# Kernel tuning notes

Measured on AMD Instinct MI355X. Metric: run time of the kernel, lower is better.

Reference implementation:

```python
import jax, jax.numpy as jnp
import numpy as np

B, C_IN, C_OUT, H, W = 4, 64, 64, 64, 64
D = 2 * C_OUT  # projected channel dim = 128


def conv1x1(x, w, b):
    # x: [B,Cin,H,W], w: [Cout,Cin], b: [Cout]
    return jnp.einsum('bchw,oc->bohw', x, w) + b[None, :, None, None]


def setup_inputs() -> dict:
    key = jax.random.key(0)
    ks = jax.random.split(key, 10)
    s_q = 1.0 / np.sqrt(C_IN)
    s_kv = 1.0 / np.sqrt(2 * C_IN)
    s_o = 1.0 / np.sqrt(D)
    return {
        'x_upper': jax.random.normal(ks[0], (B, C_IN, H, W), jnp.float32),
        'x_lower': jax.random.normal(ks[1], (B, 2 * C_IN, H, W), jnp.float32),
        'wq': jax.random.uniform(ks[2], (D, C_IN), jnp.float32, -s_q, s_q),
        'bq': jax.random.uniform(ks[3], (D,), jnp.float32, -s_q, s_q),
        'wk': jax.random.uniform(ks[4], (D, 2 * C_IN), jnp.float32, -s_kv, s_kv),
        'bk': jax.random.uniform(ks[5], (D,), jnp.float32, -s_kv, s_kv),
        'wv': jax.random.uniform(ks[6], (D, 2 * C_IN), jnp.float32, -s_kv, s_kv),
        'bv': jax.random.uniform(ks[7], (D,), jnp.float32, -s_kv, s_kv),
        'wo': jax.random.uniform(ks[8], (D, D), jnp.float32, -s_o, s_o),
        'bo': jax.random.uniform(ks[9], (D,), jnp.float32, -s_o, s_o),
    }


def reference(x_upper, x_lower, wq, bq, wk, bk, wv, bv, wo, bo):
    q = conv1x1(x_upper, wq, bq)   # [B,D,H,W]
    k = conv1x1(x_lower, wk, bk)   # [B,D,H,W]
    v = conv1x1(x_lower, wv, bv)   # [B,D,H,W]
    b, d = q.shape[0], q.shape[1]
    # NOTE: the torch code uses .view (raw reshape), NOT a transpose --
    # faithful translation is a plain reshape of the contiguous NCHW tensor.
    qf = q.reshape(b, -1, d)       # [B, N, D], N = H*W
    kf = k.reshape(b, -1, d)
    vf = v.reshape(b, -1, d)
    scores = jnp.einsum('bnd,bmd->bnm', qf, kf) / (d ** 0.5)  # [B,N,N]
    attn = jax.nn.softmax(scores, axis=-1)
    of = jnp.einsum('bnm,bmd->bnd', attn, vf)  # [B,N,D]
    out = of.reshape(v.shape)                  # [B,D,H,W]
    out = conv1x1(out, wo, bo) + x_lower
    return out
```

## Files before the change

### kernel.cpp

```cpp
#include <hip/hip_runtime.h>
#include <math.h>

#define BB 4
#define CIN 64
#define CL 128
#define DD 128
#define HW 4096
#define NN 4096
#define TP 132
#define YP 136

typedef __attribute__((ext_vector_type(8))) __bf16 bf16x8;
typedef __attribute__((ext_vector_type(16))) float f32x16;

__device__ __forceinline__ unsigned short f2bf(float f) {
    unsigned u = __builtin_bit_cast(unsigned, f);
    u += 0x7fffu + ((u >> 16) & 1u);
    return (unsigned short)(u >> 16);
}
__device__ __forceinline__ unsigned pack2(float lo, float hi) {
    return (unsigned)f2bf(lo) | ((unsigned)f2bf(hi) << 16);
}
__device__ __forceinline__ float bf2f(unsigned s) {
    return __builtin_bit_cast(float, s << 16);
}
__device__ __forceinline__ unsigned pack_trunc(float lo, float hi) {
    return __builtin_amdgcn_perm(__builtin_bit_cast(unsigned, hi),
                                 __builtin_bit_cast(unsigned, lo), 0x07060302u);
}
__device__ __forceinline__ float exp2_fast(float x) {
#if __has_builtin(__builtin_amdgcn_exp2f)
    return __builtin_amdgcn_exp2f(x);
#else
    return __expf(x * 0.6931471805599453f);
#endif
}
__device__ __forceinline__ void async_copy16(const unsigned short* g,
                                             unsigned short* l) {
    __builtin_amdgcn_global_load_lds(
        (const __attribute__((address_space(1))) void*)g,
        (__attribute__((address_space(3))) void*)l, 16, 0, 0);
}

__device__ __forceinline__ void split8(const float xv[8], bf16x8* hi, bf16x8* lo) {
    union { unsigned u[4]; bf16x8 v; } H, L;
#pragma unroll
    for (int i = 0; i < 4; ++i) {
        float x0 = xv[2 * i], x1 = xv[2 * i + 1];
        H.u[i] = pack_trunc(x0, x1);
        float h0 = __builtin_bit_cast(float,
                     __builtin_bit_cast(unsigned, x0) & 0xffff0000u);
        float h1 = __builtin_bit_cast(float,
                     __builtin_bit_cast(unsigned, x1) & 0xffff0000u);
        L.u[i] = pack_trunc(x0 - h0, x1 - h1);
    }
    *hi = H.v; *lo = L.v;
}

__global__ __launch_bounds__(512) void proj_qkv_mfma(
    const float* __restrict__ xq, const float* __restrict__ wq,
    const float* __restrict__ bq, unsigned short* __restrict__ qout,
    const float* __restrict__ xl,
    const float* __restrict__ wk, const float* __restrict__ bk,
    const float* __restrict__ wv, const float* __restrict__ bv,
    unsigned short* __restrict__ kout, unsigned short* __restrict__ vout,
    float oscale)
{
    __shared__ __align__(16) char smem[135168];
    float* xsf = (float*)smem;
    unsigned short* ytk = (unsigned short*)(smem + 65536);
    unsigned short* ytv = (unsigned short*)(smem + 100352);

    const int tid = threadIdx.x;
    const int w = tid >> 6;
    const int lane = tid & 63;
    const int half = lane >> 5;
    const int l5 = lane & 31;

    if (blockIdx.x < 128) {
        const int b = blockIdx.x >> 5;
        const int tile = blockIdx.x & 31;
        const int px0 = tile * 128;
        const int g = w >> 2;
        const int ms = w & 3;

        {
            const float* src = xl + (size_t)b * CL * HW + px0
                             + (size_t)(lane >> 5) * HW + (lane & 31) * 4;
#pragma unroll
            for (int k = 0; k < 8; ++k) {
                int c = w * 8 + k;
                async_copy16((const unsigned short*)(src + (size_t)(2 * c) * HW),
                             (unsigned short*)(smem + c * 1024));
            }
        }

        const float* wsrc = g ? wv : wk;
        const float* bsrc = g ? bv : bk;
        bf16x8 Ah[8], Al[8];
        {
            const float* wr = wsrc + (size_t)(ms * 32 + l5) * CL + half * 8;
#pragma unroll
            for (int ks = 0; ks < 8; ++ks) {
                float tmp[8];
                *(float4*)&tmp[0] = *(const float4*)(wr + ks * 16);
                *(float4*)&tmp[4] = *(const float4*)(wr + ks * 16 + 4);
                split8(tmp, &Ah[ks], &Al[ks]);
            }
        }
        float biasr[16];
#pragma unroll
        for (int r = 0; r < 16; ++r)
            biasr[r] = bsrc[ms * 32 + (r & 3) + 8 * (r >> 2) + 4 * half];

        f32x16 acc[4];
#pragma unroll
        for (int ns = 0; ns < 4; ++ns)
#pragma unroll
            for (int r = 0; r < 16; ++r) acc[ns][r] = biasr[r];

        asm volatile("s_waitcnt vmcnt(0)" ::: "memory");
        __builtin_amdgcn_s_barrier();
        asm volatile("" ::: "memory");

#pragma unroll
        for (int ns = 0; ns < 4; ++ns) {
            int pxl = ns * 32 + l5;
#pragma unroll
            for (int ks = 0; ks < 8; ++ks) {
                int kb_ = ks * 16 + half * 8;
                float xv[8];
#pragma unroll
                for (int j = 0; j < 8; ++j)
                    xv[j] = xsf[(kb_ + j) * 128 + pxl];
                bf16x8 Bh, Bl;
                split8(xv, &Bh, &Bl);
                acc[ns] = __builtin_amdgcn_mfma_f32_32x32x16_bf16(Ah[ks], Bh, acc[ns], 0, 0, 0);
                acc[ns] = __builtin_amdgcn_mfma_f32_32x32x16_bf16(Ah[ks], Bl, acc[ns], 0, 0, 0);
                acc[ns] = __builtin_amdgcn_mfma_f32_32x32x16_bf16(Al[ks], Bh, acc[ns], 0, 0, 0);
            }
        }

        unsigned short* yt = g ? ytv : ytk;
#pragma unroll
        for (int ns = 0; ns < 4; ++ns) {
            int pxl = ns * 32 + l5;
#pragma unroll
            for (int r = 0; r < 16; ++r) {
                int o = ms * 32 + (r & 3) + 8 * (r >> 2) + 4 * half;
                yt[o * YP + pxl] = f2bf(acc[ns][r]);
            }
        }
        __syncthreads();

        unsigned short* kbase = kout + (size_t)b * NN * DD;
        unsigned short* vbase = vout + (size_t)b * 128 * HW + px0;
        const int tm = tile & 15;
#pragma unroll
        for (int i = 0; i < 4; ++i) {
            int e = tid + i * 512;
            int o = e >> 4, q = e & 15;
            uint4 kq4 = *(const uint4*)(ytk + o * YP + q * 8);
            *(uint4*)(kbase + (size_t)(o * 32 + tile) * 128 + ((q ^ tm) * 8)) = kq4;
            uint4 vq4 = *(const uint4*)(ytv + o * YP + q * 8);
            *(uint4*)(vbase + (size_t)o * HW + q * 8) = vq4;
        }
    } else {
        const int qb_ = blockIdx.x - 128;
        const int b = qb_ >> 5;
        const int tile = qb_ & 31;
        const int px0 = tile * 128;
        const int ms = w & 3;
        const int nsg = w >> 2;

        {
            const float* src = xq + (size_t)b * CIN * HW + px0
                             + (size_t)(lane >> 5) * HW + (lane & 31) * 4;
#pragma unroll
            for (int k = 0; k < 4; ++k) {
                int c = w * 4 + k;
                async_copy16((const unsigned short*)(src + (size_t)(2 * c) * HW),
                             (unsigned short*)(smem + c * 1024));
            }
        }

        bf16x8 Ah[4], Al[4];
        {
            const float* wr = wq + (size_t)(ms * 32 + l5) * CIN + half * 8;
#pragma unroll
            for (int ks = 0; ks < 4; ++ks) {
                float tmp[8];
                *(float4*)&tmp[0] = *(const float4*)(wr + ks * 16);
                *(float4*)&tmp[4] = *(const float4*)(wr + ks * 16 + 4);
                split8(tmp, &Ah[ks], &Al[ks]);
            }
        }
        float biasr[16];
#pragma unroll
        for (int r = 0; r < 16; ++r)
            biasr[r] = bq[ms * 32 + (r & 3) + 8 * (r >> 2) + 4 * half];

        f32x16 acc[2];
#pragma unroll
        for (int i = 0; i < 2; ++i)
#pragma unroll
            for (int r = 0; r < 16; ++r) acc[i][r] = biasr[r];

        asm volatile("s_waitcnt vmcnt(0)" ::: "memory");
        __builtin_amdgcn_s_barrier();
        asm volatile("" ::: "memory");

#pragma unroll
        for (int i = 0; i < 2; ++i) {
            int pxl = (nsg * 2 + i) * 32 + l5;
#pragma unroll
            for (int ks = 0; ks < 4; ++ks) {
                int kb_ = ks * 16 + half * 8;
                float xv[8];
#pragma unroll
                for (int j = 0; j < 8; ++j)
                    xv[j] = xsf[(kb_ + j) * 128 + pxl];
                bf16x8 Bh, Bl;
                split8(xv, &Bh, &Bl);
                acc[i] = __builtin_amdgcn_mfma_f32_32x32x16_bf16(Ah[ks], Bh, acc[i], 0, 0, 0);
                acc[i] = __builtin_amdgcn_mfma_f32_32x32x16_bf16(Ah[ks], Bl, acc[i], 0, 0, 0);
                acc[i] = __builtin_amdgcn_mfma_f32_32x32x16_bf16(Al[ks], Bh, acc[i], 0, 0, 0);
            }
        }

#pragma unroll
        for (int i = 0; i < 2; ++i) {
            int pxl = (nsg * 2 + i) * 32 + l5;
#pragma unroll
            for (int r = 0; r < 16; ++r) {
                int o = ms * 32 + (r & 3) + 8 * (r >> 2) + 4 * half;
                ytk[o * YP + pxl] = f2bf(acc[i][r] * oscale);
            }
        }
        __syncthreads();

        unsigned short* qbase = qout + (size_t)b * 128 * HW + px0;
#pragma unroll
        for (int i = 0; i < 4; ++i) {
            int e = tid + i * 512;
            int o = e >> 4, q = e & 15;
            uint4 qq4 = *(const uint4*)(ytk + o * YP + q * 8);
            *(uint4*)(qbase + (size_t)o * HW + q * 8) = qq4;
        }
    }
}

__global__ __launch_bounds__(512) void proj_o_mfma(
    const unsigned short* __restrict__ x, const float* __restrict__ w,
    const float* __restrict__ bias, const float* __restrict__ resid,
    float* __restrict__ out)
{
    __shared__ __align__(16) unsigned short xs16[128 * 64];

    const int tid = threadIdx.x;
    const int w_ = tid >> 6;
    const int lane = tid & 63;
    const int half = lane >> 5;
    const int l5 = lane & 31;
    const int b = blockIdx.x >> 6;
    const int tile = blockIdx.x & 63;
    const int px0 = tile * 64;
    const int ms = w_ & 3;
    const int pxh = w_ >> 2;

    {
        const unsigned short* src = x + (size_t)b * DD * HW + px0
                                  + (size_t)(lane >> 3) * HW + (lane & 7) * 8;
#pragma unroll
        for (int k = 0; k < 2; ++k) {
            int c = w_ * 2 + k;
            async_copy16(src + (size_t)(8 * c) * HW, xs16 + c * 512);
        }
    }

    bf16x8 Ah[8], Al[8];
    {
        const float* wr = w + (size_t)(ms * 32 + l5) * DD + half * 8;
#pragma unroll
        for (int ks = 0; ks < 8; ++ks) {
            float tmp[8];
            *(float4*)&tmp[0] = *(const float4*)(wr + ks * 16);
            *(float4*)&tmp[4] = *(const float4*)(wr + ks * 16 + 4);
            split8(tmp, &Ah[ks], &Al[ks]);
        }
    }
    f32x16 acc;
#pragma unroll
    for (int r = 0; r < 16; ++r)
        acc[r] = bias[ms * 32 + (r & 3) + 8 * (r >> 2) + 4 * half];

    asm volatile("s_waitcnt vmcnt(0)" ::: "memory");
    __builtin_amdgcn_s_barrier();
    asm volatile("" ::: "memory");

    {
        int pxl = pxh * 32 + l5;
#pragma unroll
        for (int ks = 0; ks < 8; ++ks) {
            int kb_ = ks * 16 + half * 8;
            union { unsigned u[4]; bf16x8 v; } B;
#pragma unroll
            for (int p = 0; p < 4; ++p) {
                unsigned e0 = xs16[(kb_ + 2 * p) * 64 + pxl];
                unsigned e1 = xs16[(kb_ + 2 * p + 1) * 64 + pxl];
                B.u[p] = e0 | (e1 << 16);
            }
            acc = __builtin_amdgcn_mfma_f32_32x32x16_bf16(Ah[ks], B.v, acc, 0, 0, 0);
            acc = __builtin_amdgcn_mfma_f32_32x32x16_bf16(Al[ks], B.v, acc, 0, 0, 0);
        }
    }

    {
        int px = px0 + pxh * 32 + l5;
#pragma unroll
        for (int r = 0; r < 16; ++r) {
            int o = ms * 32 + (r & 3) + 8 * (r >> 2) + 4 * half;
            size_t a = ((size_t)b * 128 + o) * HW + px;
            out[a] = acc[r] + resid[a];
        }
    }
}

__global__ __launch_bounds__(256) void transpose_v(
    const unsigned short* __restrict__ vf, unsigned short* __restrict__ vt)
{
    __shared__ unsigned short tld[16 * TP];
    int tid = threadIdx.x;
    int b = blockIdx.x >> 8;
    int n0 = (blockIdx.x & 255) * 16;
    const unsigned short* src = vf + (size_t)b * NN * DD + (size_t)n0 * DD;
    {
        int n = tid >> 4, x = tid & 15;
        union { uint4 q; unsigned long long u[2]; } t;
        t.q = *(const uint4*)(src + (size_t)n * DD + x * 8);
        unsigned short* d = &tld[n * TP + x * 8];
        *(unsigned long long*)(d) = t.u[0];
        *(unsigned long long*)(d + 4) = t.u[1];
    }
    __syncthreads();
    unsigned short* dst = vt + (size_t)b * NN * DD + (size_t)(n0 >> 7) * 16384;
    int xb_ = (n0 & 127) >> 3;
    {
        int g = tid & 1, d = tid >> 1;
        union { uint4 q; unsigned short s[8]; } t;
#pragma unroll
        for (int j = 0; j < 8; ++j) t.s[j] = tld[(g * 8 + j) * TP + d];
        int xs = (xb_ + g) ^ (d & 15);
        *(uint4*)(dst + (size_t)d * 128 + xs * 8) = t.q;
    }
}

__global__ __launch_bounds__(512) void attn_mfma(
    const unsigned short* __restrict__ qf, const unsigned short* __restrict__ kfs,
    const unsigned short* __restrict__ vts, unsigned short* __restrict__ of)
{
    __shared__ __align__(16) char smem[133632];

    const int tid = threadIdx.x;
    const int lane = tid & 63;
    const int w = tid >> 6;
    const int kq = w & 3;
    const int rh = w >> 2;
    const int half = lane >> 5;
    const int l5 = lane & 31;
    const int b = blockIdx.x >> 6;
    const int rb0 = (blockIdx.x & 63) * 64;
    const int rw0 = rb0 + rh * 32;
    const int cw = kq * 32;

    const unsigned short* qb = qf + (size_t)b * NN * DD;
    const unsigned short* kb = kfs + (size_t)b * NN * DD;
    const unsigned short* vb = vts + (size_t)b * NN * DD;

    bf16x8 qfrag[8];
    {
        const unsigned short* qrow = qb + (size_t)(rw0 + l5) * DD + half * 8;
#pragma unroll
        for (int kk = 0; kk < 8; ++kk)
            qfrag[kk] = *(const bf16x8*)(qrow + kk * 16);
    }

    f32x16 O[4] = {};
    float lacc = 0.f;

    auto stage = [&](int t, int buf) {
        const unsigned short* kt = kb + (size_t)t * 16384;
        const unsigned short* vt_ = vb + (size_t)t * 16384;
        unsigned short* kl = (unsigned short*)(smem + buf * 65536);
        unsigned short* vl = kl + 16384;
#pragma unroll
        for (int j = 0; j < 4; ++j) {
            int c = (w * 4 + j) * 512;
            async_copy16(kt + c + lane * 8, kl + c);
            async_copy16(vt_ + c + lane * 8, vl + c);
        }
    };

    stage(0, 0);
    stage(1, 1);

    const int NT = NN / 128;
    for (int t = 0; t < NT; ++t) {
        const int cur = t & 1;
        if (t < NT - 1) asm volatile("s_waitcnt vmcnt(8)" ::: "memory");
        else            asm volatile("s_waitcnt vmcnt(0)" ::: "memory");
        __builtin_amdgcn_s_barrier();
        asm volatile("" ::: "memory");

        const unsigned short* kl = (const unsigned short*)(smem + cur * 65536);
        const unsigned short* vl = kl + 16384;

        f32x16 S = {};
        __builtin_amdgcn_s_setprio(1);
#pragma unroll
        for (int kk = 0; kk < 8; ++kk) {
            bf16x8 kfr = *(const bf16x8*)
                &kl[(cw + l5) * 128 + (((kk * 2 + half) ^ (l5 & 15)) * 8)];
            S = __builtin_amdgcn_mfma_f32_32x32x16_bf16(kfr, qfrag[kk], S, 0, 0, 0);
        }
        __builtin_amdgcn_s_setprio(0);

        float p[16];
#pragma unroll
        for (int r = 0; r < 16; ++r) p[r] = exp2_fast(S[r]);
        {
            float t0 = (p[0] + p[1]) + (p[2] + p[3]);
            float t1 = (p[4] + p[5]) + (p[6] + p[7]);
            float t2 = (p[8] + p[9]) + (p[10] + p[11]);
            float t3 = (p[12] + p[13]) + (p[14] + p[15]);
            lacc += (t0 + t1) + (t2 + t3);
        }

#pragma unroll
        for (int kc = 0; kc < 2; ++kc) {
            unsigned PA0 = pack_trunc(p[8 * kc + 0], p[8 * kc + 1]);
            unsigned PA1 = pack_trunc(p[8 * kc + 2], p[8 * kc + 3]);
            unsigned PB0 = pack_trunc(p[8 * kc + 4], p[8 * kc + 5]);
            unsigned PB1 = pack_trunc(p[8 * kc + 6], p[8 * kc + 7]);
            unsigned snd0 = half ? PA0 : PB0;
            unsigned snd1 = half ? PA1 : PB1;
            unsigned rcv0 = (unsigned)__shfl_xor((int)snd0, 32, 64);
            unsigned rcv1 = (unsigned)__shfl_xor((int)snd1, 32, 64);
            union { unsigned u[4]; bf16x8 v; } pf;
            pf.u[0] = half ? rcv0 : PA0;
            pf.u[1] = half ? rcv1 : PA1;
            pf.u[2] = half ? PB0 : rcv0;
            pf.u[3] = half ? PB1 : rcv1;
            __builtin_amdgcn_s_setprio(1);
#pragma unroll
            for (int ds = 0; ds < 4; ++ds) {
                bf16x8 vfr = *(const bf16x8*)
                    &vl[(ds * 32 + l5) * 128 +
                        (((kq * 4 + kc * 2 + half) ^ (l5 & 15)) * 8)];
                O[ds] = __builtin_amdgcn_mfma_f32_32x32x16_bf16(vfr, pf.v, O[ds], 0, 0, 0);
            }
            __builtin_amdgcn_s_setprio(0);
        }

        asm volatile("s_waitcnt lgkmcnt(0)" ::: "memory");
        __builtin_amdgcn_s_barrier();
        asm volatile("" ::: "memory");
        if (t + 2 < NT) stage(t + 2, cur);
    }

    lacc += __shfl_xor(lacc, 32, 64);

    float (*red_o)[64][129] = (float (*)[64][129])smem;
    float* red_l = (float*)(smem + 132096);
    if (half == 0) red_l[kq * 64 + rh * 32 + l5] = lacc;
#pragma unroll
    for (int ds = 0; ds < 4; ++ds)
#pragma unroll
        for (int r = 0; r < 16; ++r) {
            int d = ds * 32 + (r & 3) + 8 * (r >> 2) + 4 * half;
            red_o[kq][rh * 32 + l5][d] = O[ds][r];
        }
    __syncthreads();

    {
        int q = tid >> 3;
        int dg = tid & 7;
        float l = red_l[q] + red_l[64 + q] + red_l[128 + q] + red_l[192 + q];
        float inv = 1.f / l;
        unsigned outw[8];
#pragma unroll
        for (int i = 0; i < 8; ++i) {
            int d0 = dg * 16 + i * 2;
            float s0 = red_o[0][q][d0] + red_o[1][q][d0] +
                       red_o[2][q][d0] + red_o[3][q][d0];
            float s1 = red_o[0][q][d0 + 1] + red_o[1][q][d0 + 1] +
                       red_o[2][q][d0 + 1] + red_o[3][q][d0 + 1];
            outw[i] = pack2(s0 * inv, s1 * inv);
        }
        unsigned short* ob = of + (size_t)b * NN * DD + (size_t)(rb0 + q) * DD + dg * 16;
        *(uint4*)(ob) = *(uint4*)&outw[0];
        *(uint4*)(ob + 8) = *(uint4*)&outw[4];
    }
}

extern "C" void kernel_launch(void* const* d_in, const int* in_sizes, int n_in,
                              void* d_out, int out_size, void* d_ws, size_t ws_size,
                              hipStream_t stream) {
    const float* x_upper = (const float*)d_in[0];
    const float* x_lower = (const float*)d_in[1];
    const float* wq = (const float*)d_in[2];
    const float* bq = (const float*)d_in[3];
    const float* wk = (const float*)d_in[4];
    const float* bk = (const float*)d_in[5];
    const float* wv = (const float*)d_in[6];
    const float* bv = (const float*)d_in[7];
    const float* wo = (const float*)d_in[8];
    const float* bo = (const float*)d_in[9];
    float* out = (float*)d_out;

    const size_t ELT = (size_t)BB * NN * DD;
    unsigned short* qf  = (unsigned short*)d_ws;
    unsigned short* kfs = qf + ELT;
    unsigned short* vts = kfs + ELT;
    unsigned short* vfn = vts + ELT;
    unsigned short* ofb = vfn + ELT;

    const float qscale = (float)(0.08838834764831845 * 1.4426950408889634);

    proj_qkv_mfma<<<256, 512, 0, stream>>>(x_upper, wq, bq, qf,
                                           x_lower, wk, bk, wv, bv,
                                           kfs, vfn, qscale);
    transpose_v<<<1024, 256, 0, stream>>>(vfn, vts);
    attn_mfma<<<BB * 64, 512, 0, stream>>>(qf, kfs, vts, ofb);
    proj_o_mfma<<<256, 512, 0, stream>>>(ofb, wo, bo, x_lower, out);
}
```

Measured before the change: 150.3 us.

## Fuse all four kernels into one cooperative kernel with grid syncs

Merges the QKV projection, V transpose, attention and output projection into a single cooperative launch of 256 blocks, separated by grid.sync barriers with threadfences. The transpose stage is remapped so each of the 256 blocks handles 64 rows instead of launching 1024 small blocks. The aim is to remove kernel launch gaps and per-kernel ramp overhead. In exchange, grid-wide barriers add synchronisation cost, and the large shared-memory footprint limits residency to one block per CU.

```diff
diff --git a/kernel.cpp b/kernel.cpp
--- a/kernel.cpp
+++ b/kernel.cpp
@@ -1,5 +1,8 @@
 #include <hip/hip_runtime.h>
+#include <hip/hip_cooperative_groups.h>
 #include <math.h>
+
+namespace cg = cooperative_groups;
 
 #define BB 4
 #define CIN 64
@@ -57,49 +60,410 @@
     *hi = H.v; *lo = L.v;
 }
 
-__global__ __launch_bounds__(512) void proj_qkv_mfma(
+__global__ __launch_bounds__(512) void fused_all(
     const float* __restrict__ xq, const float* __restrict__ wq,
     const float* __restrict__ bq, unsigned short* __restrict__ qout,
     const float* __restrict__ xl,
     const float* __restrict__ wk, const float* __restrict__ bk,
     const float* __restrict__ wv, const float* __restrict__ bv,
-    unsigned short* __restrict__ kout, unsigned short* __restrict__ vout,
-    float oscale)
+    unsigned short* __restrict__ kout, unsigned short* __restrict__ vfn,
+    unsigned short* __restrict__ vts, unsigned short* __restrict__ ofb,
+    const float* __restrict__ wo, const float* __restrict__ bo,
+    float* __restrict__ out, float oscale)
 {
     __shared__ __align__(16) char smem[135168];
-    float* xsf = (float*)smem;
-    unsigned short* ytk = (unsigned short*)(smem + 65536);
-    unsigned short* ytv = (unsigned short*)(smem + 100352);
-
+
+    cg::grid_group grid = cg::this_grid();
+    const int blk = blockIdx.x;
     const int tid = threadIdx.x;
-    const int w = tid >> 6;
-    const int lane = tid & 63;
-    const int half = lane >> 5;
-    const int l5 = lane & 31;
-
-    if (blockIdx.x < 128) {
-        const int b = blockIdx.x >> 5;
-        const int tile = blockIdx.x & 31;
-        const int px0 = tile * 128;
-        const int g = w >> 2;
-        const int ms = w & 3;
-
+
+    {
+        float* xsf = (float*)smem;
+        unsigned short* ytk = (unsigned short*)(smem + 65536);
+        unsigned short* ytv = (unsigned short*)(smem + 100352);
+        const int w = tid >> 6;
+        const int lane = tid & 63;
+        const int half = lane >> 5;
+        const int l5 = lane & 31;
+
+        if (blk < 128) {
+            const int b = blk >> 5;
+            const int tile = blk & 31;
+            const int px0 = tile * 128;
+            const int g = w >> 2;
+            const int ms = w & 3;
+
+            {
+                const float* src = xl + (size_t)b * CL * HW + px0
+                                 + (size_t)(lane >> 5) * HW + (lane & 31) * 4;
+#pragma unroll
+                for (int k = 0; k < 8; ++k) {
+                    int c = w * 8 + k;
+                    async_copy16((const unsigned short*)(src + (size_t)(2 * c) * HW),
+                                 (unsigned short*)(smem + c * 1024));
+                }
+            }
+
+            const float* wsrc = g ? wv : wk;
+            const float* bsrc = g ? bv : bk;
+            bf16x8 Ah[8], Al[8];
+            {
+                const float* wr = wsrc + (size_t)(ms * 32 + l5) * CL + half * 8;
+#pragma unroll
+                for (int ks = 0; ks < 8; ++ks) {
+                    float tmp[8];
+                    *(float4*)&tmp[0] = *(const float4*)(wr + ks * 16);
+                    *(float4*)&tmp[4] = *(const float4*)(wr + ks * 16 + 4);
+                    split8(tmp, &Ah[ks], &Al[ks]);
+                }
+            }
+            float biasr[16];
+#pragma unroll
+            for (int r = 0; r < 16; ++r)
+                biasr[r] = bsrc[ms * 32 + (r & 3) + 8 * (r >> 2) + 4 * half];
+
+            f32x16 acc[4];
+#pragma unroll
+            for (int ns = 0; ns < 4; ++ns)
+#pragma unroll
+                for (int r = 0; r < 16; ++r) acc[ns][r] = biasr[r];
+
+            asm volatile("s_waitcnt vmcnt(0)" ::: "memory");
+            __builtin_amdgcn_s_barrier();
+            asm volatile("" ::: "memory");
+
+#pragma unroll
+            for (int ns = 0; ns < 4; ++ns) {
+                int pxl = ns * 32 + l5;
+#pragma unroll
+                for (int ks = 0; ks < 8; ++ks) {
+                    int kb_ = ks * 16 + half * 8;
+                    float xv[8];
+#pragma unroll
+                    for (int j = 0; j < 8; ++j)
+                        xv[j] = xsf[(kb_ + j) * 128 + pxl];
+                    bf16x8 Bh, Bl;
+                    split8(xv, &Bh, &Bl);
+                    acc[ns] = __builtin_amdgcn_mfma_f32_32x32x16_bf16(Ah[ks], Bh, acc[ns], 0, 0, 0);
+                    acc[ns] = __builtin_amdgcn_mfma_f32_32x32x16_bf16(Ah[ks], Bl, acc[ns], 0, 0, 0);
+                    acc[ns] = __builtin_amdgcn_mfma_f32_32x32x16_bf16(Al[ks], Bh, acc[ns], 0, 0, 0);
+                }
+            }
+
+            unsigned short* yt = g ? ytv : ytk;
+#pragma unroll
+            for (int ns = 0; ns < 4; ++ns) {
+                int pxl = ns * 32 + l5;
+#pragma unroll
+                for (int r = 0; r < 16; ++r) {
+                    int o = ms * 32 + (r & 3) + 8 * (r >> 2) + 4 * half;
+                    yt[o * YP + pxl] = f2bf(acc[ns][r]);
+                }
+            }
+            __syncthreads();
+
+            unsigned short* kbase = kout + (size_t)b * NN * DD;
+            unsigned short* vbase = vfn + (size_t)b * 128 * HW + px0;
+            const int tm = tile & 15;
+#pragma unroll
+            for (int i = 0; i < 4; ++i) {
+                int e = tid + i * 512;
+                int o = e >> 4, q = e & 15;
+                uint4 kq4 = *(const uint4*)(ytk + o * YP + q * 8);
+                *(uint4*)(kbase + (size_t)(o * 32 + tile) * 128 + ((q ^ tm) * 8)) = kq4;
+                uint4 vq4 = *(const uint4*)(ytv + o * YP + q * 8);
+                *(uint4*)(vbase + (size_t)o * HW + q * 8) = vq4;
+            }
+        } else {
+            const int qb_ = blk - 128;
+            const int b = qb_ >> 5;
+            const int tile = qb_ & 31;
+            const int px0 = tile * 128;
+            const int ms = w & 3;
+            const int nsg = w >> 2;
+
+            {
+                const float* src = xq + (size_t)b * CIN * HW + px0
+                                 + (size_t)(lane >> 5) * HW + (lane & 31) * 4;
+#pragma unroll
+                for (int k = 0; k < 4; ++k) {
+                    int c = w * 4 + k;
+                    async_copy16((const unsigned short*)(src + (size_t)(2 * c) * HW),
+                                 (unsigned short*)(smem + c * 1024));
+                }
+            }
+
+            bf16x8 Ah[4], Al[4];
+            {
+                const float* wr = wq + (size_t)(ms * 32 + l5) * CIN + half * 8;
+#pragma unroll
+                for (int ks = 0; ks < 4; ++ks) {
+                    float tmp[8];
+                    *(float4*)&tmp[0] = *(const float4*)(wr + ks * 16);
+                    *(float4*)&tmp[4] = *(const float4*)(wr + ks * 16 + 4);
+                    split8(tmp, &Ah[ks], &Al[ks]);
+                }
+            }
+            float biasr[16];
+#pragma unroll
+            for (int r = 0; r < 16; ++r)
+                biasr[r] = bq[ms * 32 + (r & 3) + 8 * (r >> 2) + 4 * half];
+
+            f32x16 acc[2];
+#pragma unroll
+            for (int i = 0; i < 2; ++i)
+#pragma unroll
+                for (int r = 0; r < 16; ++r) acc[i][r] = biasr[r];
+
+            asm volatile("s_waitcnt vmcnt(0)" ::: "memory");
+            __builtin_amdgcn_s_barrier();
+            asm volatile("" ::: "memory");
+
+#pragma unroll
+            for (int i = 0; i < 2; ++i) {
+                int pxl = (nsg * 2 + i) * 32 + l5;
+#pragma unroll
+                for (int ks = 0; ks < 4; ++ks) {
+                    int kb_ = ks * 16 + half * 8;
+                    float xv[8];
+#pragma unroll
+                    for (int j = 0; j < 8; ++j)
+                        xv[j] = xsf[(kb_ + j) * 128 + pxl];
+                    bf16x8 Bh, Bl;
+                    split8(xv, &Bh, &Bl);
+                    acc[i] = __builtin_amdgcn_mfma_f32_32x32x16_bf16(Ah[ks], Bh, acc[i], 0, 0, 0);
+                    acc[i] = __builtin_amdgcn_mfma_f32_32x32x16_bf16(Ah[ks], Bl, acc[i], 0, 0, 0);
+                    acc[i] = __builtin_amdgcn_mfma_f32_32x32x16_bf16(Al[ks], Bh, acc[i], 0, 0, 0);
+                }
+            }
+
+#pragma unroll
+            for (int i = 0; i < 2; ++i) {
+                int pxl = (nsg * 2 + i) * 32 + l5;
+#pragma unroll
+                for (int r = 0; r < 16; ++r) {
+                    int o = ms * 32 + (r & 3) + 8 * (r >> 2) + 4 * half;
+                    ytk[o * YP + pxl] = f2bf(acc[i][r] * oscale);
+                }
+            }
+            __syncthreads();
+
+            unsigned short* qbase = qout + (size_t)b * 128 * HW + px0;
+#pragma unroll
+            for (int i = 0; i < 4; ++i) {
+                int e = tid + i * 512;
+                int o = e >> 4, q = e & 15;
+                uint4 qq4 = *(const uint4*)(ytk + o * YP + q * 8);
+                *(uint4*)(qbase + (size_t)o * HW + q * 8) = qq4;
+            }
+        }
+    }
+    __threadfence();
+    grid.sync();
+
+    {
+        unsigned short* tld = (unsigned short*)smem;
+        const int b = blk >> 6;
+        const int n0 = (blk & 63) * 64;
+        const unsigned short* src = vfn + (size_t)b * NN * DD + (size_t)n0 * DD;
+#pragma unroll
+        for (int i = 0; i < 2; ++i) {
+            int ch = tid + i * 512;
+            int n = ch >> 4, x = ch & 15;
+            union { uint4 q; unsigned long long u[2]; } t;
+            t.q = *(const uint4*)(src + (size_t)n * DD + x * 8);
+            unsigned short* d = &tld[n * TP + x * 8];
+            *(unsigned long long*)(d) = t.u[0];
+            *(unsigned long long*)(d + 4) = t.u[1];
+        }
+        __syncthreads();
+        unsigned short* dst = vts + (size_t)b * NN * DD + (size_t)(n0 >> 7) * 16384;
+        int xb_ = (n0 & 127) >> 3;
+#pragma unroll
+        for (int i = 0; i < 2; ++i) {
+            int ch = tid + i * 512;
+            int g = ch & 7, d = ch >> 3;
+            union { uint4 q; unsigned short s[8]; } t;
+#pragma unroll
+            for (int j = 0; j < 8; ++j) t.s[j] = tld[(g * 8 + j) * TP + d];
+            int xs = (xb_ + g) ^ (d & 15);
+            *(uint4*)(dst + (size_t)d * 128 + xs * 8) = t.q;
+        }
+        __syncthreads();
+    }
+    __threadfence();
+    grid.sync();
+
+    {
+        const int lane = tid & 63;
+        const int w = tid >> 6;
+        const int kq = w & 3;
+        const int rh = w >> 2;
+        const int half = lane >> 5;
+        const int l5 = lane & 31;
+        const int b = blk >> 6;
+        const int rb0 = (blk & 63) * 64;
+        const int rw0 = rb0 + rh * 32;
+        const int cw = kq * 32;
+
+        const unsigned short* qb = qout + (size_t)b * NN * DD;
+        const unsigned short* kb = kout + (size_t)b * NN * DD;
+        const unsigned short* vb = vts + (size_t)b * NN * DD;
+
+        bf16x8 qfrag[8];
         {
-            const float* src = xl + (size_t)b * CL * HW + px0
-                             + (size_t)(lane >> 5) * HW + (lane & 31) * 4;
-#pragma unroll
-            for (int k = 0; k < 8; ++k) {
-                int c = w * 8 + k;
-                async_copy16((const unsigned short*)(src + (size_t)(2 * c) * HW),
-                             (unsigned short*)(smem + c * 1024));
-            }
-        }
-
-        const float* wsrc = g ? wv : wk;
-        const float* bsrc = g ? bv : bk;
+            const unsigned short* qrow = qb + (size_t)(rw0 + l5) * DD + half * 8;
+#pragma unroll
+            for (int kk = 0; kk < 8; ++kk)
+                qfrag[kk] = *(const bf16x8*)(qrow + kk * 16);
+        }
+
+        f32x16 O[4] = {};
+        float lacc = 0.f;
+
+        auto stage = [&](int t, int buf) {
+            const unsigned short* kt = kb + (size_t)t * 16384;
+            const unsigned short* vt_ = vb + (size_t)t * 16384;
+            unsigned short* kl = (unsigned short*)(smem + buf * 65536);
+            unsigned short* vl = kl + 16384;
+#pragma unroll
+            for (int j = 0; j < 4; ++j) {
+                int c = (w * 4 + j) * 512;
+                async_copy16(kt + c + lane * 8, kl + c);
+                async_copy16(vt_ + c + lane * 8, vl + c);
+            }
+        };
+
+        stage(0, 0);
+        stage(1, 1);
+
+        const int NT = NN / 128;
+        for (int t = 0; t < NT; ++t) {
+            const int cur = t & 1;
+            if (t < NT - 1) asm volatile("s_waitcnt vmcnt(8)" ::: "memory");
+            else            asm volatile("s_waitcnt vmcnt(0)" ::: "memory");
+            __builtin_amdgcn_s_barrier();
+            asm volatile("" ::: "memory");
+
+            const unsigned short* kl = (const unsigned short*)(smem + cur * 65536);
+            const unsigned short* vl = kl + 16384;
+
+            f32x16 S = {};
+            __builtin_amdgcn_s_setprio(1);
+#pragma unroll
+            for (int kk = 0; kk < 8; ++kk) {
+                bf16x8 kfr = *(const bf16x8*)
+                    &kl[(cw + l5) * 128 + (((kk * 2 + half) ^ (l5 & 15)) * 8)];
+                S = __builtin_amdgcn_mfma_f32_32x32x16_bf16(kfr, qfrag[kk], S, 0, 0, 0);
+            }
+            __builtin_amdgcn_s_setprio(0);
+
+            float p[16];
+#pragma unroll
+            for (int r = 0; r < 16; ++r) p[r] = exp2_fast(S[r]);
+            {
+                float t0 = (p[0] + p[1]) + (p[2] + p[3]);
+                float t1 = (p[4] + p[5]) + (p[6] + p[7]);
+                float t2 = (p[8] + p[9]) + (p[10] + p[11]);
+                float t3 = (p[12] + p[13]) + (p[14] + p[15]);
+                lacc += (t0 + t1) + (t2 + t3);
+            }
+
+#pragma unroll
+            for (int kc = 0; kc < 2; ++kc) {
+                unsigned PA0 = pack_trunc(p[8 * kc + 0], p[8 * kc + 1]);
+                unsigned PA1 = pack_trunc(p[8 * kc + 2], p[8 * kc + 3]);
+                unsigned PB0 = pack_trunc(p[8 * kc + 4], p[8 * kc + 5]);
+                unsigned PB1 = pack_trunc(p[8 * kc + 6], p[8 * kc + 7]);
+                unsigned snd0 = half ? PA0 : PB0;
+                unsigned snd1 = half ? PA1 : PB1;
+                unsigned rcv0 = (unsigned)__shfl_xor((int)snd0, 32, 64);
+                unsigned rcv1 = (unsigned)__shfl_xor((int)snd1, 32, 64);
+                union { unsigned u[4]; bf16x8 v; } pf;
+                pf.u[0] = half ? rcv0 : PA0;
+                pf.u[1] = half ? rcv1 : PA1;
+                pf.u[2] = half ? PB0 : rcv0;
+                pf.u[3] = half ? PB1 : rcv1;
+                __builtin_amdgcn_s_setprio(1);
+#pragma unroll
+                for (int ds = 0; ds < 4; ++ds) {
+                    bf16x8 vfr = *(const bf16x8*)
+                        &vl[(ds * 32 + l5) * 128 +
+                            (((kq * 4 + kc * 2 + half) ^ (l5 & 15)) * 8)];
+                    O[ds] = __builtin_amdgcn_mfma_f32_32x32x16_bf16(vfr, pf.v, O[ds], 0, 0, 0);
+                }
+                __builtin_amdgcn_s_setprio(0);
+            }
+
+            asm volatile("s_waitcnt lgkmcnt(0)" ::: "memory");
+            __builtin_amdgcn_s_barrier();
+            asm volatile("" ::: "memory");
+            if (t + 2 < NT) stage(t + 2, cur);
+        }
+
+        lacc += __shfl_xor(lacc, 32, 64);
+
+        float (*red_o)[64][129] = (float (*)[64][129])smem;
+        float* red_l = (float*)(smem + 132096);
+        if (half == 0) red_l[kq * 64 + rh * 32 + l5] = lacc;
+#pragma unroll
+        for (int ds = 0; ds < 4; ++ds)
+#pragma unroll
+            for (int r = 0; r < 16; ++r) {
+                int d = ds * 32 + (r & 3) + 8 * (r >> 2) + 4 * half;
+                red_o[kq][rh * 32 + l5][d] = O[ds][r];
+            }
+        __syncthreads();
+
+        {
+            int q = tid >> 3;
+            int dg = tid & 7;
+            float l = red_l[q] + red_l[64 + q] + red_l[128 + q] + red_l[192 + q];
+            float inv = 1.f / l;
+            unsigned outw[8];
+#pragma unroll
+            for (int i = 0; i < 8; ++i) {
+                int d0 = dg * 16 + i * 2;
+                float s0 = red_o[0][q][d0] + red_o[1][q][d0] +
+                           red_o[2][q][d0] + red_o[3][q][d0];
+                float s1 = red_o[0][q][d0 + 1] + red_o[1][q][d0 + 1] +
+                           red_o[2][q][d0 + 1] + red_o[3][q][d0 + 1];
+                outw[i] = pack2(s0 * inv, s1 * inv);
+            }
+            unsigned short* ob = ofb + (size_t)b * NN * DD + (size_t)(rb0 + q) * DD + dg * 16;
+            *(uint4*)(ob) = *(uint4*)&outw[0];
+            *(uint4*)(ob + 8) = *(uint4*)&outw[4];
+        }
+        __syncthreads();
+    }
+    __threadfence();
+    grid.sync();
+
+    {
+        unsigned short* xs16 = (unsigned short*)smem;
+        const int w_ = tid >> 6;
+        const int lane = tid & 63;
+        const int half = lane >> 5;
+        const int l5 = lane & 31;
+        const int b = blk >> 6;
+        const int tile = blk & 63;
+        const int px0 = tile * 64;
+        const int ms = w_ & 3;
+        const int pxh = w_ >> 2;
+
+        {
+            const unsigned short* src = ofb + (size_t)b * DD * HW + px0
+                                      + (size_t)(lane >> 3) * HW + (lane & 7) * 8;
+#pragma unroll
+            for (int k = 0; k < 2; ++k) {
+                int c = w_ * 2 + k;
+                async_copy16(src + (size_t)(8 * c) * HW, xs16 + c * 512);
+            }
+        }
+
         bf16x8 Ah[8], Al[8];
         {
-            const float* wr = wsrc + (size_t)(ms * 32 + l5) * CL + half * 8;
+            const float* wr = wo + (size_t)(ms * 32 + l5) * DD + half * 8;
 #pragma unroll
             for (int ks = 0; ks < 8; ++ks) {
                 float tmp[8];
@@ -108,398 +472,41 @@
                 split8(tmp, &Ah[ks], &Al[ks]);
             }
         }
-        float biasr[16];
+        f32x16 acc;
 #pragma unroll
         for (int r = 0; r < 16; ++r)
-            biasr[r] = bsrc[ms * 32 + (r & 3) + 8 * (r >> 2) + 4 * half];
-
-        f32x16 acc[4];
-#pragma unroll
-        for (int ns = 0; ns < 4; ++ns)
-#pragma unroll
-            for (int r = 0; r < 16; ++r) acc[ns][r] = biasr[r];
+            acc[r] = bo[ms * 32 + (r & 3) + 8 * (r >> 2) + 4 * half];
 
         asm volatile("s_waitcnt vmcnt(0)" ::: "memory");
         __builtin_amdgcn_s_barrier();
         asm volatile("" ::: "memory");
 
-#pragma unroll
-        for (int ns = 0; ns < 4; ++ns) {
-            int pxl = ns * 32 + l5;
+        {
+            int pxl = pxh * 32 + l5;
 #pragma unroll
             for (int ks = 0; ks < 8; ++ks) {
                 int kb_ = ks * 16 + half * 8;
-                float xv[8];
-#pragma unroll
-                for (int j = 0; j < 8; ++j)
-                    xv[j] = xsf[(kb_ + j) * 128 + pxl];
-                bf16x8 Bh, Bl;
-                split8(xv, &Bh, &Bl);
-                acc[ns] = __builtin_amdgcn_mfma_f32_32x32x16_bf16(Ah[ks], Bh, acc[ns], 0, 0, 0);
-                acc[ns] = __builtin_amdgcn_mfma_f32_32x32x16_bf16(Ah[ks], Bl, acc[ns], 0, 0, 0);
-                acc[ns] = __builtin_amdgcn_mfma_f32_32x32x16_bf16(Al[ks], Bh, acc[ns], 0, 0, 0);
-            }
-        }
-
-        unsigned short* yt = g ? ytv : ytk;
-#pragma unroll
-        for (int ns = 0; ns < 4; ++ns) {
-            int pxl = ns * 32 + l5;
+                union { unsigned u[4]; bf16x8 v; } B;
+#pragma unroll
+                for (int p = 0; p < 4; ++p) {
+                    unsigned e0 = xs16[(kb_ + 2 * p) * 64 + pxl];
+                    unsigned e1 = xs16[(kb_ + 2 * p + 1) * 64 + pxl];
+                    B.u[p] = e0 | (e1 << 16);
+                }
+                acc = __builtin_amdgcn_mfma_f32_32x32x16_bf16(Ah[ks], B.v, acc, 0, 0, 0);
+                acc = __builtin_amdgcn_mfma_f32_32x32x16_bf16(Al[ks], B.v, acc, 0, 0, 0);
+            }
+        }
+
+        {
+            int px = px0 + pxh * 32 + l5;
 #pragma unroll
             for (int r = 0; r < 16; ++r) {
                 int o = ms * 32 + (r & 3) + 8 * (r >> 2) + 4 * half;
-                yt[o * YP + pxl] = f2bf(acc[ns][r]);
-            }
-        }
-        __syncthreads();
-
-        unsigned short* kbase = kout + (size_t)b * NN * DD;
-        unsigned short* vbase = vout + (size_t)b * 128 * HW + px0;
-        const int tm = tile & 15;
-#pragma unroll
-        for (int i = 0; i < 4; ++i) {
-            int e = tid + i * 512;
-            int o = e >> 4, q = e & 15;
-            uint4 kq4 = *(const uint4*)(ytk + o * YP + q * 8);
-            *(uint4*)(kbase + (size_t)(o * 32 + tile) * 128 + ((q ^ tm) * 8)) = kq4;
-            uint4 vq4 = *(const uint4*)(ytv + o * YP + q * 8);
-            *(uint4*)(vbase + (size_t)o * HW + q * 8) = vq4;
-        }
-    } else {
-        const int qb_ = blockIdx.x - 128;
-        const int b = qb_ >> 5;
-        const int tile = qb_ & 31;
-        const int px0 = tile * 128;
-        const int ms = w & 3;
-        const int nsg = w >> 2;
-
-        {
-            const float* src = xq + (size_t)b * CIN * HW + px0
-                             + (size_t)(lane >> 5) * HW + (lane & 31) * 4;
-#pragma unroll
-            for (int k = 0; k < 4; ++k) {
-                int c = w * 4 + k;
-                async_copy16((const unsigned short*)(src + (size_t)(2 * c) * HW),
-                             (unsigned short*)(smem + c * 1024));
-            }
-        }
-
-        bf16x8 Ah[4], Al[4];
-        {
-            const float* wr = wq + (size_t)(ms * 32 + l5) * CIN + half * 8;
-#pragma unroll
-            for (int ks = 0; ks < 4; ++ks) {
-                float tmp[8];
-                *(float4*)&tmp[0] = *(const float4*)(wr + ks * 16);
-                *(float4*)&tmp[4] = *(const float4*)(wr + ks * 16 + 4);
-                split8(tmp, &Ah[ks], &Al[ks]);
-            }
-        }
-        float biasr[16];
-#pragma unroll
-        for (int r = 0; r < 16; ++r)
-            biasr[r] = bq[ms * 32 + (r & 3) + 8 * (r >> 2) + 4 * half];
-
-        f32x16 acc[2];
-#pragma unroll
-        for (int i = 0; i < 2; ++i)
-#pragma unroll
-            for (int r = 0; r < 16; ++r) acc[i][r] = biasr[r];
-
-        asm volatile("s_waitcnt vmcnt(0)" ::: "memory");
-        __builtin_amdgcn_s_barrier();
-        asm volatile("" ::: "memory");
-
-#pragma unroll
-        for (int i = 0; i < 2; ++i) {
-            int pxl = (nsg * 2 + i) * 32 + l5;
-#pragma unroll
-            for (int ks = 0; ks < 4; ++ks) {
-                int kb_ = ks * 16 + half * 8;
-                float xv[8];
-#pragma unroll
-                for (int j = 0; j < 8; ++j)
-                    xv[j] = xsf[(kb_ + j) * 128 + pxl];
-                bf16x8 Bh, Bl;
-                split8(xv, &Bh, &Bl);
-                acc[i] = __builtin_amdgcn_mfma_f32_32x32x16_bf16(Ah[ks], Bh, acc[i], 0, 0, 0);
-                acc[i] = __builtin_amdgcn_mfma_f32_32x32x16_bf16(Ah[ks], Bl, acc[i], 0, 0, 0);
-                acc[i] = __builtin_amdgcn_mfma_f32_32x32x16_bf16(Al[ks], Bh, acc[i], 0, 0, 0);
-            }
-        }
-
-#pragma unroll
-        for (int i = 0; i < 2; ++i) {
-            int pxl = (nsg * 2 + i) * 32 + l5;
-#pragma unroll
-            for (int r = 0; r < 16; ++r) {
-                int o = ms * 32 + (r & 3) + 8 * (r >> 2) + 4 * half;
-                ytk[o * YP + pxl] = f2bf(acc[i][r] * oscale);
-            }
-        }
-        __syncthreads();
-
-        unsigned short* qbase = qout + (size_t)b * 128 * HW + px0;
-#pragma unroll
-        for (int i = 0; i < 4; ++i) {
-            int e = tid + i * 512;
-            int o = e >> 4, q = e & 15;
-            uint4 qq4 = *(const uint4*)(ytk + o * YP + q * 8);
-            *(uint4*)(qbase + (size_t)o * HW + q * 8) = qq4;
-        }
-    }
-}
-
-__global__ __launch_bounds__(512) void proj_o_mfma(
-    const unsigned short* __restrict__ x, const float* __restrict__ w,
-    const float* __restrict__ bias, const float* __restrict__ resid,
-    float* __restrict__ out)
-{
-    __shared__ __align__(16) unsigned short xs16[128 * 64];
-
-    const int tid = threadIdx.x;
-    const int w_ = tid >> 6;
-    const int lane = tid & 63;
-    const int half = lane >> 5;
-    const int l5 = lane & 31;
-    const int b = blockIdx.x >> 6;
-    const int tile = blockIdx.x & 63;
-    const int px0 = tile * 64;
-    const int ms = w_ & 3;
-    const int pxh = w_ >> 2;
-
-    {
-        const unsigned short* src = x + (size_t)b * DD * HW + px0
-                                  + (size_t)(lane >> 3) * HW + (lane & 7) * 8;
-#pragma unroll
-        for (int k = 0; k < 2; ++k) {
-            int c = w_ * 2 + k;
-            async_copy16(src + (size_t)(8 * c) * HW, xs16 + c * 512);
-        }
-    }
-
-    bf16x8 Ah[8], Al[8];
-    {
-        const float* wr = w + (size_t)(ms * 32 + l5) * DD + half * 8;
-#pragma unroll
-        for (int ks = 0; ks < 8; ++ks) {
-            float tmp[8];
-            *(float4*)&tmp[0] = *(const float4*)(wr + ks * 16);
-            *(float4*)&tmp[4] = *(const float4*)(wr + ks * 16 + 4);
-            split8(tmp, &Ah[ks], &Al[ks]);
-        }
-    }
-    f32x16 acc;
-#pragma unroll
-    for (int r = 0; r < 16; ++r)
-        acc[r] = bias[ms * 32 + (r & 3) + 8 * (r >> 2) + 4 * half];
-
-    asm volatile("s_waitcnt vmcnt(0)" ::: "memory");
-    __builtin_amdgcn_s_barrier();
-    asm volatile("" ::: "memory");
-
-    {
-        int pxl = pxh * 32 + l5;
-#pragma unroll
-        for (int ks = 0; ks < 8; ++ks) {
-            int kb_ = ks * 16 + half * 8;
-            union { unsigned u[4]; bf16x8 v; } B;
-#pragma unroll
-            for (int p = 0; p < 4; ++p) {
-                unsigned e0 = xs16[(kb_ + 2 * p) * 64 + pxl];
-                unsigned e1 = xs16[(kb_ + 2 * p + 1) * 64 + pxl];
-                B.u[p] = e0 | (e1 << 16);
-            }
-            acc = __builtin_amdgcn_mfma_f32_32x32x16_bf16(Ah[ks], B.v, acc, 0, 0, 0);
-            acc = __builtin_amdgcn_mfma_f32_32x32x16_bf16(Al[ks], B.v, acc, 0, 0, 0);
-        }
-    }
-
-    {
-        int px = px0 + pxh * 32 + l5;
-#pragma unroll
-        for (int r = 0; r < 16; ++r) {
-            int o = ms * 32 + (r & 3) + 8 * (r >> 2) + 4 * half;
-            size_t a = ((size_t)b * 128 + o) * HW + px;
-            out[a] = acc[r] + resid[a];
-        }
-    }
-}
-
-__global__ __launch_bounds__(256) void transpose_v(
-    const unsigned short* __restrict__ vf, unsigned short* __restrict__ vt)
-{
-    __shared__ unsigned short tld[16 * TP];
-    int tid = threadIdx.x;
-    int b = blockIdx.x >> 8;
-    int n0 = (blockIdx.x & 255) * 16;
-    const unsigned short* src = vf + (size_t)b * NN * DD + (size_t)n0 * DD;
-    {
-        int n = tid >> 4, x = tid & 15;
-        union { uint4 q; unsigned long long u[2]; } t;
-        t.q = *(const uint4*)(src + (size_t)n * DD + x * 8);
-        unsigned short* d = &tld[n * TP + x * 8];
-        *(unsigned long long*)(d) = t.u[0];
-        *(unsigned long long*)(d + 4) = t.u[1];
-    }
-    __syncthreads();
-    unsigned short* dst = vt + (size_t)b * NN * DD + (size_t)(n0 >> 7) * 16384;
-    int xb_ = (n0 & 127) >> 3;
-    {
-        int g = tid & 1, d = tid >> 1;
-        union { uint4 q; unsigned short s[8]; } t;
-#pragma unroll
-        for (int j = 0; j < 8; ++j) t.s[j] = tld[(g * 8 + j) * TP + d];
-        int xs = (xb_ + g) ^ (d & 15);
-        *(uint4*)(dst + (size_t)d * 128 + xs * 8) = t.q;
-    }
-}
-
-__global__ __launch_bounds__(512) void attn_mfma(
-    const unsigned short* __restrict__ qf, const unsigned short* __restrict__ kfs,
-    const unsigned short* __restrict__ vts, unsigned short* __restrict__ of)
-{
-    __shared__ __align__(16) char smem[133632];
-
-    const int tid = threadIdx.x;
-    const int lane = tid & 63;
-    const int w = tid >> 6;
-    const int kq = w & 3;
-    const int rh = w >> 2;
-    const int half = lane >> 5;
-    const int l5 = lane & 31;
-    const int b = blockIdx.x >> 6;
-    const int rb0 = (blockIdx.x & 63) * 64;
-    const int rw0 = rb0 + rh * 32;
-    const int cw = kq * 32;
-
-    const unsigned short* qb = qf + (size_t)b * NN * DD;
-    const unsigned short* kb = kfs + (size_t)b * NN * DD;
-    const unsigned short* vb = vts + (size_t)b * NN * DD;
-
-    bf16x8 qfrag[8];
-    {
-        const unsigned short* qrow = qb + (size_t)(rw0 + l5) * DD + half * 8;
-#pragma unroll
-        for (int kk = 0; kk < 8; ++kk)
-            qfrag[kk] = *(const bf16x8*)(qrow + kk * 16);
-    }
-
-    f32x16 O[4] = {};
-    float lacc = 0.f;
-
-    auto stage = [&](int t, int buf) {
-        const unsigned short* kt = kb + (size_t)t * 16384;
-        const unsigned short* vt_ = vb + (size_t)t * 16384;
-        unsigned short* kl = (unsigned short*)(smem + buf * 65536);
-        unsigned short* vl = kl + 16384;
-#pragma unroll
-        for (int j = 0; j < 4; ++j) {
-            int c = (w * 4 + j) * 512;
-            async_copy16(kt + c + lane * 8, kl + c);
-            async_copy16(vt_ + c + lane * 8, vl + c);
-        }
-    };
-
-    stage(0, 0);
-    stage(1, 1);
-
-    const int NT = NN / 128;
-    for (int t = 0; t < NT; ++t) {
-        const int cur = t & 1;
-        if (t < NT - 1) asm volatile("s_waitcnt vmcnt(8)" ::: "memory");
-        else            asm volatile("s_waitcnt vmcnt(0)" ::: "memory");
-        __builtin_amdgcn_s_barrier();
-        asm volatile("" ::: "memory");
-
-        const unsigned short* kl = (const unsigned short*)(smem + cur * 65536);
-        const unsigned short* vl = kl + 16384;
-
-        f32x16 S = {};
-        __builtin_amdgcn_s_setprio(1);
-#pragma unroll
-        for (int kk = 0; kk < 8; ++kk) {
-            bf16x8 kfr = *(const bf16x8*)
-                &kl[(cw + l5) * 128 + (((kk * 2 + half) ^ (l5 & 15)) * 8)];
-            S = __builtin_amdgcn_mfma_f32_32x32x16_bf16(kfr, qfrag[kk], S, 0, 0, 0);
-        }
-        __builtin_amdgcn_s_setprio(0);
-
-        float p[16];
-#pragma unroll
-        for (int r = 0; r < 16; ++r) p[r] = exp2_fast(S[r]);
-        {
-            float t0 = (p[0] + p[1]) + (p[2] + p[3]);
-            float t1 = (p[4] + p[5]) + (p[6] + p[7]);
-            float t2 = (p[8] + p[9]) + (p[10] + p[11]);
-            float t3 = (p[12] + p[13]) + (p[14] + p[15]);
-            lacc += (t0 + t1) + (t2 + t3);
-        }
-
-#pragma unroll
-        for (int kc = 0; kc < 2; ++kc) {
-            unsigned PA0 = pack_trunc(p[8 * kc + 0], p[8 * kc + 1]);
-            unsigned PA1 = pack_trunc(p[8 * kc + 2], p[8 * kc + 3]);
-            unsigned PB0 = pack_trunc(p[8 * kc + 4], p[8 * kc + 5]);
-            unsigned PB1 = pack_trunc(p[8 * kc + 6], p[8 * kc + 7]);
-            unsigned snd0 = half ? PA0 : PB0;
-            unsigned snd1 = half ? PA1 : PB1;
-            unsigned rcv0 = (unsigned)__shfl_xor((int)snd0, 32, 64);
-            unsigned rcv1 = (unsigned)__shfl_xor((int)snd1, 32, 64);
-            union { unsigned u[4]; bf16x8 v; } pf;
-            pf.u[0] = half ? rcv0 : PA0;
-            pf.u[1] = half ? rcv1 : PA1;
-            pf.u[2] = half ? PB0 : rcv0;
-            pf.u[3] = half ? PB1 : rcv1;
-            __builtin_amdgcn_s_setprio(1);
-#pragma unroll
-            for (int ds = 0; ds < 4; ++ds) {
-                bf16x8 vfr = *(const bf16x8*)
-                    &vl[(ds * 32 + l5) * 128 +
-                        (((kq * 4 + kc * 2 + half) ^ (l5 & 15)) * 8)];
-                O[ds] = __builtin_amdgcn_mfma_f32_32x32x16_bf16(vfr, pf.v, O[ds], 0, 0, 0);
-            }
-            __builtin_amdgcn_s_setprio(0);
-        }
-
-        asm volatile("s_waitcnt lgkmcnt(0)" ::: "memory");
-        __builtin_amdgcn_s_barrier();
-        asm volatile("" ::: "memory");
-        if (t + 2 < NT) stage(t + 2, cur);
-    }
-
-    lacc += __shfl_xor(lacc, 32, 64);
-
-    float (*red_o)[64][129] = (float (*)[64][129])smem;
-    float* red_l = (float*)(smem + 132096);
-    if (half == 0) red_l[kq * 64 + rh * 32 + l5] = lacc;
-#pragma unroll
-    for (int ds = 0; ds < 4; ++ds)
-#pragma unroll
-        for (int r = 0; r < 16; ++r) {
-            int d = ds * 32 + (r & 3) + 8 * (r >> 2) + 4 * half;
-            red_o[kq][rh * 32 + l5][d] = O[ds][r];
-        }
-    __syncthreads();
-
-    {
-        int q = tid >> 3;
-        int dg = tid & 7;
-        float l = red_l[q] + red_l[64 + q] + red_l[128 + q] + red_l[192 + q];
-        float inv = 1.f / l;
-        unsigned outw[8];
-#pragma unroll
-        for (int i = 0; i < 8; ++i) {
-            int d0 = dg * 16 + i * 2;
-            float s0 = red_o[0][q][d0] + red_o[1][q][d0] +
-                       red_o[2][q][d0] + red_o[3][q][d0];
-            float s1 = red_o[0][q][d0 + 1] + red_o[1][q][d0 + 1] +
-                       red_o[2][q][d0 + 1] + red_o[3][q][d0 + 1];
-            outw[i] = pack2(s0 * inv, s1 * inv);
-        }
-        unsigned short* ob = of + (size_t)b * NN * DD + (size_t)(rb0 + q) * DD + dg * 16;
-        *(uint4*)(ob) = *(uint4*)&outw[0];
-        *(uint4*)(ob + 8) = *(uint4*)&outw[4];
+                size_t a = ((size_t)b * 128 + o) * HW + px;
+                out[a] = acc[r] + xl[a];
+            }
+        }
     }
 }
 
@@ -525,12 +532,14 @@
     unsigned short* vfn = vts + ELT;
     unsigned short* ofb = vfn + ELT;
 
-    const float qscale = (float)(0.08838834764831845 * 1.4426950408889634);
-
-    proj_qkv_mfma<<<256, 512, 0, stream>>>(x_upper, wq, bq, qf,
-                                           x_lower, wk, bk, wv, bv,
-                                           kfs, vfn, qscale);
-    transpose_v<<<1024, 256, 0, stream>>>(vfn, vts);
-    attn_mfma<<<BB * 64, 512, 0, stream>>>(qf, kfs, vts, ofb);
-    proj_o_mfma<<<256, 512, 0, stream>>>(ofb, wo, bo, x_lower, out);
-}
+    float qscale = (float)(0.08838834764831845 * 1.4426950408889634);
+
+    void* args[] = {
+        (void*)&x_upper, (void*)&wq, (void*)&bq, (void*)&qf,
+        (void*)&x_lower, (void*)&wk, (void*)&bk, (void*)&wv, (void*)&bv,
+        (void*)&kfs, (void*)&vfn, (void*)&vts, (void*)&ofb,
+        (void*)&wo, (void*)&bo, (void*)&out, (void*)&qscale
+    };
+    hipLaunchCooperativeKernel((void*)fused_all, dim3(256), dim3(512),
+                               args, 0, stream);
+}
```

Measured after the change: 399.2 us. 2.66x slower.
